# Performance work log

Measured on AMD Instinct MI355X. Metric: run time of the kernel, lower is better.

The kernel has to match this reference:

```python
import jax, jax.numpy as jnp
import numpy as np

N_NODES = 50000
N_EDGES = 800000
IN_DIM = 128
OUT_DIM = 64


def setup_inputs() -> dict:
    key = jax.random.key(0)
    k1, k2, k3, k4, k5 = jax.random.split(key, 5)
    x = jax.random.normal(k1, (N_NODES, IN_DIM), dtype=jnp.float32)
    edge_src = jax.random.randint(k2, (N_EDGES,), 0, N_NODES, dtype=jnp.int64)
    edge_dst = jax.random.randint(k3, (N_EDGES,), 0, N_NODES, dtype=jnp.int64)
    edge_weight = jax.random.uniform(k4, (N_EDGES,), dtype=jnp.float32)
    # Glorot-uniform weight as in weight_variable_glorot (range = sqrt(6/input_dim))
    init_range = np.sqrt(6.0 / IN_DIM).astype(np.float32)
    w = jax.random.uniform(k5, (IN_DIM, OUT_DIM), minval=-init_range,
                           maxval=init_range, dtype=jnp.float32)
    return {"x": x, "edge_src": edge_src, "edge_dst": edge_dst,
            "edge_weight": edge_weight, "w": w}


def reference(x, edge_src, edge_dst, edge_weight, w):
    # Dense projection: [N, in] @ [in, out] -> [N, out]
    h = x @ w
    # Sparse adjacency matmul (adj @ h) in COO form:
    # out[dst] += weight * h[src]
    msgs = edge_weight[:, None] * h[edge_src]          # [E, out]
    agg = jax.ops.segment_sum(msgs, edge_dst, num_segments=N_NODES)
    return jax.nn.relu(agg)
```

## Files before the change

kernel.cpp:

```cpp
#include <hip/hip_runtime.h>

#define N_NODES 50000
#define N_EDGES 800000
#define IN_DIM 128
#define OUT_DIM 64
#define ROWS 64
#define NB 782
#define CHUNK 8192
#define NCH ((N_EDGES + CHUNK - 1) / CHUNK)
#define SCAN_N (NB * NCH)
#define SCAN_BLK 512
#define NSC ((SCAN_N + SCAN_BLK - 1) / SCAN_BLK)

__device__ __forceinline__ unsigned short f2bf(float f) {
    unsigned u = __builtin_bit_cast(unsigned, f);
    u += 0x7FFF + ((u >> 16) & 1);
    return (unsigned short)(u >> 16);
}
__device__ __forceinline__ float bf2f(unsigned short u) {
    unsigned x = ((unsigned)u) << 16;
    return __builtin_bit_cast(float, x);
}

__global__ __launch_bounds__(256, 2) void gc_gemm(const float* __restrict__ x,
                                                  const float* __restrict__ w,
                                                  unsigned short* __restrict__ h16) {
    __shared__ float w_lds[IN_DIM * OUT_DIM];
    __shared__ float x_lds[ROWS * IN_DIM];

    const int tid = threadIdx.x;
    const int row0 = blockIdx.x * ROWS;

    const float4* w4 = reinterpret_cast<const float4*>(w);
    float4* wl4 = reinterpret_cast<float4*>(w_lds);
#pragma unroll
    for (int i = 0; i < 8; ++i) wl4[tid + i * 256] = w4[tid + i * 256];

    const float4* x4 = reinterpret_cast<const float4*>(x);
    float4* xl4 = reinterpret_cast<float4*>(x_lds);
#pragma unroll
    for (int i = 0; i < 8; ++i) {
        const int idx = tid + i * 256;
        const int r = idx >> 5;
        const int kc = idx & 31;
        const int g = row0 + r;
        float4 v = make_float4(0.f, 0.f, 0.f, 0.f);
        if (g < N_NODES) v = x4[(size_t)g * 32 + kc];
        xl4[r * 32 + (kc ^ (r & 3))] = v;
    }
    __syncthreads();

    const int tx = tid & 15;
    const int ty = tid >> 4;
    const int sw = ty & 3;

    float4 acc[4];
#pragma unroll
    for (int i = 0; i < 4; ++i) acc[i] = make_float4(0.f, 0.f, 0.f, 0.f);

    for (int kc = 0; kc < 32; ++kc) {
        float4 xv[4], wv[4];
#pragma unroll
        for (int i = 0; i < 4; ++i)
            xv[i] = xl4[(ty + 16 * i) * 32 + (kc ^ sw)];
#pragma unroll
        for (int j = 0; j < 4; ++j)
            wv[j] = wl4[(kc * 4 + j) * 16 + tx];
#pragma unroll
        for (int i = 0; i < 4; ++i) {
            acc[i].x = fmaf(xv[i].x, wv[0].x, acc[i].x);
            acc[i].y = fmaf(xv[i].x, wv[0].y, acc[i].y);
            acc[i].z = fmaf(xv[i].x, wv[0].z, acc[i].z);
            acc[i].w = fmaf(xv[i].x, wv[0].w, acc[i].w);
            acc[i].x = fmaf(xv[i].y, wv[1].x, acc[i].x);
            acc[i].y = fmaf(xv[i].y, wv[1].y, acc[i].y);
            acc[i].z = fmaf(xv[i].y, wv[1].z, acc[i].z);
            acc[i].w = fmaf(xv[i].y, wv[1].w, acc[i].w);
            acc[i].x = fmaf(xv[i].z, wv[2].x, acc[i].x);
            acc[i].y = fmaf(xv[i].z, wv[2].y, acc[i].y);
            acc[i].z = fmaf(xv[i].z, wv[2].z, acc[i].z);
            acc[i].w = fmaf(xv[i].z, wv[2].w, acc[i].w);
            acc[i].x = fmaf(xv[i].w, wv[3].x, acc[i].x);
            acc[i].y = fmaf(xv[i].w, wv[3].y, acc[i].y);
            acc[i].z = fmaf(xv[i].w, wv[3].z, acc[i].z);
            acc[i].w = fmaf(xv[i].w, wv[3].w, acc[i].w);
        }
    }

    ushort4* h4 = reinterpret_cast<ushort4*>(h16);
#pragma unroll
    for (int i = 0; i < 4; ++i) {
        const int r = row0 + ty + 16 * i;
        if (r < N_NODES) {
            ushort4 o;
            o.x = f2bf(acc[i].x);
            o.y = f2bf(acc[i].y);
            o.z = f2bf(acc[i].z);
            o.w = f2bf(acc[i].w);
            h4[(size_t)r * 16 + tx] = o;
        }
    }
}

__global__ __launch_bounds__(512) void gc_count(const int* __restrict__ edst,
                                                int* __restrict__ cntT) {
    __shared__ int lh[NB];
    const int t = threadIdx.x;
    for (int i = t; i < NB; i += 512) lh[i] = 0;
    __syncthreads();
    const int base = blockIdx.x * CHUNK;
#pragma unroll
    for (int k = 0; k < 16; ++k) {
        const int e = base + k * 512 + t;
        if (e < N_EDGES) atomicAdd(&lh[edst[e] >> 6], 1);
    }
    __syncthreads();
    for (int i = t; i < NB; i += 512) cntT[i * NCH + blockIdx.x] = lh[i];
}

__global__ __launch_bounds__(256) void gc_scan1(const int* __restrict__ a,
                                                int* __restrict__ bsum) {
    __shared__ int red[256];
    const int t = threadIdx.x;
    const int i0 = blockIdx.x * SCAN_BLK + t * 2;
    int v = 0;
    if (i0 < SCAN_N) v += a[i0];
    if (i0 + 1 < SCAN_N) v += a[i0 + 1];
    red[t] = v;
    __syncthreads();
#pragma unroll
    for (int s = 128; s > 0; s >>= 1) {
        if (t < s) red[t] += red[t + s];
        __syncthreads();
    }
    if (t == 0) bsum[blockIdx.x] = red[0];
}

__global__ __launch_bounds__(256) void gc_scan2(int* __restrict__ bsum) {
    __shared__ int part[256];
    const int t = threadIdx.x;
    const int v = (t < NSC) ? bsum[t] : 0;
    part[t] = v;
    __syncthreads();
#pragma unroll
    for (int off = 1; off < 256; off <<= 1) {
        const int u = (t >= off) ? part[t - off] : 0;
        __syncthreads();
        part[t] += u;
        __syncthreads();
    }
    if (t < NSC) bsum[t] = part[t] - v;
}

__global__ __launch_bounds__(256) void gc_scan3(int* __restrict__ a,
                                                const int* __restrict__ bsum) {
    __shared__ int part[256];
    const int t = threadIdx.x;
    const int i0 = blockIdx.x * SCAN_BLK + t * 2;
    const int v0 = (i0 < SCAN_N) ? a[i0] : 0;
    const int v1 = (i0 + 1 < SCAN_N) ? a[i0 + 1] : 0;
    const int s = v0 + v1;
    part[t] = s;
    __syncthreads();
#pragma unroll
    for (int off = 1; off < 256; off <<= 1) {
        const int u = (t >= off) ? part[t - off] : 0;
        __syncthreads();
        part[t] += u;
        __syncthreads();
    }
    const int pre = bsum[blockIdx.x] + part[t] - s;
    if (i0 < SCAN_N) a[i0] = pre;
    if (i0 + 1 < SCAN_N) a[i0 + 1] = pre + v0;
}

__global__ __launch_bounds__(512) void gc_bin(const int* __restrict__ esrc,
                                              const int* __restrict__ edst,
                                              const float* __restrict__ ew,
                                              const int* __restrict__ posT,
                                              int2* __restrict__ tmp) {
    __shared__ int2 stage[CHUNK];
    __shared__ int lh[NB];
    __shared__ int lbase[NB];
    __shared__ int lcur[NB];
    __shared__ int part[512];

    const int t = threadIdx.x;
    const int base = blockIdx.x * CHUNK;

    for (int i = t; i < NB; i += 512) lh[i] = 0;
    __syncthreads();

#pragma unroll
    for (int k = 0; k < 16; ++k) {
        const int e = base + k * 512 + t;
        if (e < N_EDGES) atomicAdd(&lh[edst[e] >> 6], 1);
    }
    __syncthreads();

    {
        int s = 0;
        if (t < 391) s = lh[2 * t] + lh[2 * t + 1];
        part[t] = s;
        __syncthreads();
#pragma unroll
        for (int off = 1; off < 512; off <<= 1) {
            const int u = (t >= off) ? part[t - off] : 0;
            __syncthreads();
            part[t] += u;
            __syncthreads();
        }
        if (t < 391) {
            const int pre = part[t] - s;
            lbase[2 * t] = pre;
            lcur[2 * t] = pre;
            lbase[2 * t + 1] = pre + lh[2 * t];
            lcur[2 * t + 1] = pre + lh[2 * t];
        }
    }
    __syncthreads();

#pragma unroll
    for (int k = 0; k < 16; ++k) {
        const int e = base + k * 512 + t;
        if (e < N_EDGES) {
            const int d = edst[e];
            const int p = atomicAdd(&lcur[d >> 6], 1);
            stage[p] = make_int2((int)(((unsigned)(d & 63) << 16) | (unsigned)esrc[e]),
                                 __float_as_int(ew[e]));
        }
    }
    __syncthreads();

    const int wv = t >> 6, ln = t & 63;
    for (int b = wv; b < NB; b += 8) {
        const int cnt = lh[b];
        if (!cnt) continue;
        const int gbase = posT[b * NCH + blockIdx.x];
        const int lb = lbase[b];
        for (int i = ln; i < cnt; i += 64) tmp[gbase + i] = stage[lb + i];
    }
}

__global__ __launch_bounds__(256) void gc_bagg(const unsigned short* __restrict__ h16,
                                               const int* __restrict__ posT,
                                               const int2* __restrict__ tmp,
                                               float* __restrict__ out) {
    __shared__ float tiles[4 * 64 * 64];
    const int t = threadIdx.x;
    const int b = blockIdx.x;
    const int wv = t >> 6;
    const int ln = t & 63;

    for (int i = t; i < 4 * 4096; i += 256) tiles[i] = 0.f;
    __syncthreads();

    float* tile = &tiles[wv * 4096];

    const int beg = posT[b * NCH];
    const int end = (b + 1 < NB) ? posT[(b + 1) * NCH] : N_EDGES;
    const int cnt = end - beg;
    const int wbeg = beg + ((cnt * wv) >> 2);
    const int wend = beg + ((cnt * (wv + 1)) >> 2);
    const int wcnt = wend - wbeg;
    const int nfull = wcnt & ~7;

    for (int jj = 0; jj < nfull; jj += 8) {
        const int j = wbeg + jj;
        int2 rec[8];
#pragma unroll
        for (int i = 0; i < 8; ++i) rec[i] = tmp[j + i];
        float hv[8];
#pragma unroll
        for (int i = 0; i < 8; ++i) {
            const int src = rec[i].x & 0xFFFF;
            hv[i] = bf2f(h16[(size_t)src * OUT_DIM + ln]);
        }
#pragma unroll
        for (int i = 0; i < 8; ++i) {
            const int row = (rec[i].x >> 16) & 63;
            tile[row * 64 + ln] += __int_as_float(rec[i].y) * hv[i];
        }
    }
    for (int jj = nfull; jj < wcnt; ++jj) {
        const int2 r = tmp[wbeg + jj];
        const int src = r.x & 0xFFFF;
        const int row = (r.x >> 16) & 63;
        tile[row * 64 + ln] += __int_as_float(r.y) * bf2f(h16[(size_t)src * OUT_DIM + ln]);
    }
    __syncthreads();

    const int node0 = b * 64;
    float4* o4 = reinterpret_cast<float4*>(out);
    const float4* t4 = reinterpret_cast<const float4*>(tiles);
    for (int i = t; i < 1024; i += 256) {
        const float4 a = t4[i];
        const float4 b2 = t4[1024 + i];
        const float4 c = t4[2048 + i];
        const float4 d = t4[3072 + i];
        float4 s;
        s.x = fmaxf(a.x + b2.x + c.x + d.x, 0.f);
        s.y = fmaxf(a.y + b2.y + c.y + d.y, 0.f);
        s.z = fmaxf(a.z + b2.z + c.z + d.z, 0.f);
        s.w = fmaxf(a.w + b2.w + c.w + d.w, 0.f);
        const int r = i >> 4;
        const int gn = node0 + r;
        if (gn < N_NODES) o4[(size_t)gn * 16 + (i & 15)] = s;
    }
}

extern "C" void kernel_launch(void* const* d_in, const int* in_sizes, int n_in,
                              void* d_out, int out_size, void* d_ws, size_t ws_size,
                              hipStream_t stream) {
    const float* x    = (const float*)d_in[0];
    const int*   esrc = (const int*)d_in[1];
    const int*   edst = (const int*)d_in[2];
    const float* ew   = (const float*)d_in[3];
    const float* w    = (const float*)d_in[4];
    float* out = (float*)d_out;

    unsigned short* h16 = (unsigned short*)d_ws;
    int*  cntT = (int*)(h16 + (size_t)N_NODES * OUT_DIM);
    int*  bsum = cntT + 76800;
    int2* tmp  = (int2*)(bsum + 256);

    gc_gemm<<<(N_NODES + ROWS - 1) / ROWS, 256, 0, stream>>>(x, w, h16);

    gc_count<<<NCH, 512, 0, stream>>>(edst, cntT);
    gc_scan1<<<NSC, 256, 0, stream>>>(cntT, bsum);
    gc_scan2<<<1, 256, 0, stream>>>(bsum);
    gc_scan3<<<NSC, 256, 0, stream>>>(cntT, bsum);
    gc_bin<<<NCH, 512, 0, stream>>>(esrc, edst, ew, cntT, tmp);

    gc_bagg<<<NB, 256, 0, stream>>>(h16, cntT, tmp, out);
}
```

Baseline: 219.7 us.

## Split each 64-node bucket into four sub-buckets to interleave independent edge streams

```diff
diff --git a/kernel.cpp b/kernel.cpp
--- a/kernel.cpp
+++ b/kernel.cpp
@@ -6,10 +6,11 @@
 #define OUT_DIM 64
 #define ROWS 64
 #define NB 782
-#define CHUNK 8192
+#define NB4 (NB * 4)
+#define CHUNK 4096
 #define NCH ((N_EDGES + CHUNK - 1) / CHUNK)
-#define SCAN_N (NB * NCH)
-#define SCAN_BLK 512
+#define SCAN_N (NB4 * NCH)
+#define SCAN_BLK 1024
 #define NSC ((SCAN_N + SCAN_BLK - 1) / SCAN_BLK)
 
 __device__ __forceinline__ unsigned short f2bf(float f) {
@@ -104,28 +105,32 @@
 
 __global__ __launch_bounds__(512) void gc_count(const int* __restrict__ edst,
                                                 int* __restrict__ cntT) {
-    __shared__ int lh[NB];
-    const int t = threadIdx.x;
-    for (int i = t; i < NB; i += 512) lh[i] = 0;
+    __shared__ int lh[NB4];
+    const int t = threadIdx.x;
+    for (int i = t; i < NB4; i += 512) lh[i] = 0;
     __syncthreads();
     const int base = blockIdx.x * CHUNK;
 #pragma unroll
-    for (int k = 0; k < 16; ++k) {
-        const int e = base + k * 512 + t;
-        if (e < N_EDGES) atomicAdd(&lh[edst[e] >> 6], 1);
-    }
-    __syncthreads();
-    for (int i = t; i < NB; i += 512) cntT[i * NCH + blockIdx.x] = lh[i];
+    for (int kk = 0; kk < CHUNK / 512; ++kk) {
+        const int e = base + kk * 512 + t;
+        if (e < N_EDGES) {
+            const int d = edst[e];
+            atomicAdd(&lh[((d >> 6) << 2) | (d & 3)], 1);
+        }
+    }
+    __syncthreads();
+    for (int i = t; i < NB4; i += 512) cntT[i * NCH + blockIdx.x] = lh[i];
 }
 
 __global__ __launch_bounds__(256) void gc_scan1(const int* __restrict__ a,
                                                 int* __restrict__ bsum) {
     __shared__ int red[256];
     const int t = threadIdx.x;
-    const int i0 = blockIdx.x * SCAN_BLK + t * 2;
+    const int i0 = blockIdx.x * SCAN_BLK + t * 4;
     int v = 0;
-    if (i0 < SCAN_N) v += a[i0];
-    if (i0 + 1 < SCAN_N) v += a[i0 + 1];
+#pragma unroll
+    for (int j = 0; j < 4; ++j)
+        if (i0 + j < SCAN_N) v += a[i0 + j];
     red[t] = v;
     __syncthreads();
 #pragma unroll
@@ -136,14 +141,14 @@
     if (t == 0) bsum[blockIdx.x] = red[0];
 }
 
-__global__ __launch_bounds__(256) void gc_scan2(int* __restrict__ bsum) {
-    __shared__ int part[256];
+__global__ __launch_bounds__(1024) void gc_scan2(int* __restrict__ bsum) {
+    __shared__ int part[1024];
     const int t = threadIdx.x;
     const int v = (t < NSC) ? bsum[t] : 0;
     part[t] = v;
     __syncthreads();
 #pragma unroll
-    for (int off = 1; off < 256; off <<= 1) {
+    for (int off = 1; off < 1024; off <<= 1) {
         const int u = (t >= off) ? part[t - off] : 0;
         __syncthreads();
         part[t] += u;
@@ -156,10 +161,14 @@
                                                 const int* __restrict__ bsum) {
     __shared__ int part[256];
     const int t = threadIdx.x;
-    const int i0 = blockIdx.x * SCAN_BLK + t * 2;
-    const int v0 = (i0 < SCAN_N) ? a[i0] : 0;
-    const int v1 = (i0 + 1 < SCAN_N) ? a[i0 + 1] : 0;
-    const int s = v0 + v1;
+    const int i0 = blockIdx.x * SCAN_BLK + t * 4;
+    int v[4];
+    int s = 0;
+#pragma unroll
+    for (int j = 0; j < 4; ++j) {
+        v[j] = (i0 + j < SCAN_N) ? a[i0 + j] : 0;
+        s += v[j];
+    }
     part[t] = s;
     __syncthreads();
 #pragma unroll
@@ -169,9 +178,12 @@
         part[t] += u;
         __syncthreads();
     }
-    const int pre = bsum[blockIdx.x] + part[t] - s;
-    if (i0 < SCAN_N) a[i0] = pre;
-    if (i0 + 1 < SCAN_N) a[i0 + 1] = pre + v0;
+    int run = bsum[blockIdx.x] + part[t] - s;
+#pragma unroll
+    for (int j = 0; j < 4; ++j) {
+        if (i0 + j < SCAN_N) a[i0 + j] = run;
+        run += v[j];
+    }
 }
 
 __global__ __launch_bounds__(512) void gc_bin(const int* __restrict__ esrc,
@@ -180,27 +192,30 @@
                                               const int* __restrict__ posT,
                                               int2* __restrict__ tmp) {
     __shared__ int2 stage[CHUNK];
-    __shared__ int lh[NB];
-    __shared__ int lbase[NB];
-    __shared__ int lcur[NB];
+    __shared__ int lh[NB4];
+    __shared__ int lcur[NB4];
+    __shared__ int gpos[NB4];
     __shared__ int part[512];
 
     const int t = threadIdx.x;
-    const int base = blockIdx.x * CHUNK;
-
-    for (int i = t; i < NB; i += 512) lh[i] = 0;
-    __syncthreads();
-
-#pragma unroll
-    for (int k = 0; k < 16; ++k) {
-        const int e = base + k * 512 + t;
-        if (e < N_EDGES) atomicAdd(&lh[edst[e] >> 6], 1);
+    const int blk = blockIdx.x;
+    const int base = blk * CHUNK;
+
+    for (int i = t; i < NB4; i += 512) {
+        const int f = i * NCH + blk;
+        const int p = posT[f];
+        const int pn = (f + 1 < SCAN_N) ? posT[f + 1] : N_EDGES;
+        gpos[i] = p;
+        lh[i] = pn - p;
     }
     __syncthreads();
 
     {
+        const int b0 = t * 7;
         int s = 0;
-        if (t < 391) s = lh[2 * t] + lh[2 * t + 1];
+#pragma unroll
+        for (int j = 0; j < 7; ++j)
+            if (b0 + j < NB4) s += lh[b0 + j];
         part[t] = s;
         __syncthreads();
 #pragma unroll
@@ -210,22 +225,24 @@
             part[t] += u;
             __syncthreads();
         }
-        if (t < 391) {
-            const int pre = part[t] - s;
-            lbase[2 * t] = pre;
-            lcur[2 * t] = pre;
-            lbase[2 * t + 1] = pre + lh[2 * t];
-            lcur[2 * t + 1] = pre + lh[2 * t];
-        }
-    }
-    __syncthreads();
-
-#pragma unroll
-    for (int k = 0; k < 16; ++k) {
-        const int e = base + k * 512 + t;
+        int run = part[t] - s;
+#pragma unroll
+        for (int j = 0; j < 7; ++j) {
+            if (b0 + j < NB4) {
+                lcur[b0 + j] = run;
+                run += lh[b0 + j];
+            }
+        }
+    }
+    __syncthreads();
+
+#pragma unroll
+    for (int kk = 0; kk < CHUNK / 512; ++kk) {
+        const int e = base + kk * 512 + t;
         if (e < N_EDGES) {
             const int d = edst[e];
-            const int p = atomicAdd(&lcur[d >> 6], 1);
+            const int bc = ((d >> 6) << 2) | (d & 3);
+            const int p = atomicAdd(&lcur[bc], 1);
             stage[p] = make_int2((int)(((unsigned)(d & 63) << 16) | (unsigned)esrc[e]),
                                  __float_as_int(ew[e]));
         }
@@ -233,11 +250,11 @@
     __syncthreads();
 
     const int wv = t >> 6, ln = t & 63;
-    for (int b = wv; b < NB; b += 8) {
-        const int cnt = lh[b];
+    for (int bc = wv; bc < NB4; bc += 8) {
+        const int cnt = lh[bc];
         if (!cnt) continue;
-        const int gbase = posT[b * NCH + blockIdx.x];
-        const int lb = lbase[b];
+        const int gbase = gpos[bc];
+        const int lb = lcur[bc] - cnt;
         for (int i = ln; i < cnt; i += 64) tmp[gbase + i] = stage[lb + i];
     }
 }
@@ -257,37 +274,81 @@
 
     float* tile = &tiles[wv * 4096];
 
-    const int beg = posT[b * NCH];
-    const int end = (b + 1 < NB) ? posT[(b + 1) * NCH] : N_EDGES;
-    const int cnt = end - beg;
-    const int wbeg = beg + ((cnt * wv) >> 2);
-    const int wend = beg + ((cnt * (wv + 1)) >> 2);
-    const int wcnt = wend - wbeg;
-    const int nfull = wcnt & ~7;
-
-    for (int jj = 0; jj < nfull; jj += 8) {
-        const int j = wbeg + jj;
-        int2 rec[8];
-#pragma unroll
-        for (int i = 0; i < 8; ++i) rec[i] = tmp[j + i];
-        float hv[8];
-#pragma unroll
-        for (int i = 0; i < 8; ++i) {
-            const int src = rec[i].x & 0xFFFF;
-            hv[i] = bf2f(h16[(size_t)src * OUT_DIM + ln]);
-        }
-#pragma unroll
-        for (int i = 0; i < 8; ++i) {
-            const int row = (rec[i].x >> 16) & 63;
-            tile[row * 64 + ln] += __int_as_float(rec[i].y) * hv[i];
-        }
-    }
-    for (int jj = nfull; jj < wcnt; ++jj) {
-        const int2 r = tmp[wbeg + jj];
-        const int src = r.x & 0xFFFF;
-        const int row = (r.x >> 16) & 63;
-        tile[row * 64 + ln] += __int_as_float(r.y) * bf2f(h16[(size_t)src * OUT_DIM + ln]);
-    }
+    const int f0 = (b * 4) * NCH;
+    const int s0 = posT[f0];
+    const int s1 = posT[f0 + NCH];
+    const int s2 = posT[f0 + 2 * NCH];
+    const int s3 = posT[f0 + 3 * NCH];
+    const int s4 = (b * 4 + 4 < NB4) ? posT[f0 + 4 * NCH] : N_EDGES;
+    const int c0 = s1 - s0, c1 = s2 - s1, c2 = s3 - s2, c3 = s4 - s3;
+    const int jb0 = s0 + ((c0 * wv) >> 2), je0 = s0 + ((c0 * (wv + 1)) >> 2);
+    const int jb1 = s1 + ((c1 * wv) >> 2), je1 = s1 + ((c1 * (wv + 1)) >> 2);
+    const int jb2 = s2 + ((c2 * wv) >> 2), je2 = s2 + ((c2 * (wv + 1)) >> 2);
+    const int jb3 = s3 + ((c3 * wv) >> 2), je3 = s3 + ((c3 * (wv + 1)) >> 2);
+
+    const int n0 = je0 - jb0, n1 = je1 - jb1, n2 = je2 - jb2, n3 = je3 - jb3;
+    const int n = min(min(n0, n1), min(n2, n3));
+
+    int k = 0;
+    for (; k + 2 <= n; k += 2) {
+        const int2 r0 = tmp[jb0 + k];
+        const int2 r1 = tmp[jb1 + k];
+        const int2 r2 = tmp[jb2 + k];
+        const int2 r3 = tmp[jb3 + k];
+        const int2 r4 = tmp[jb0 + k + 1];
+        const int2 r5 = tmp[jb1 + k + 1];
+        const int2 r6 = tmp[jb2 + k + 1];
+        const int2 r7 = tmp[jb3 + k + 1];
+        const float h0 = bf2f(h16[(size_t)(r0.x & 0xFFFF) * OUT_DIM + ln]);
+        const float h1 = bf2f(h16[(size_t)(r1.x & 0xFFFF) * OUT_DIM + ln]);
+        const float h2 = bf2f(h16[(size_t)(r2.x & 0xFFFF) * OUT_DIM + ln]);
+        const float h3 = bf2f(h16[(size_t)(r3.x & 0xFFFF) * OUT_DIM + ln]);
+        const float h4 = bf2f(h16[(size_t)(r4.x & 0xFFFF) * OUT_DIM + ln]);
+        const float h5 = bf2f(h16[(size_t)(r5.x & 0xFFFF) * OUT_DIM + ln]);
+        const float h6 = bf2f(h16[(size_t)(r6.x & 0xFFFF) * OUT_DIM + ln]);
+        const float h7 = bf2f(h16[(size_t)(r7.x & 0xFFFF) * OUT_DIM + ln]);
+        {
+            float* p0 = &tile[((r0.x >> 16) & 63) * 64 + ln];
+            float* p1 = &tile[((r1.x >> 16) & 63) * 64 + ln];
+            float* p2 = &tile[((r2.x >> 16) & 63) * 64 + ln];
+            float* p3 = &tile[((r3.x >> 16) & 63) * 64 + ln];
+            const float a0 = *p0;
+            const float a1 = *p1;
+            const float a2 = *p2;
+            const float a3 = *p3;
+            *p0 = fmaf(__int_as_float(r0.y), h0, a0);
+            *p1 = fmaf(__int_as_float(r1.y), h1, a1);
+            *p2 = fmaf(__int_as_float(r2.y), h2, a2);
+            *p3 = fmaf(__int_as_float(r3.y), h3, a3);
+        }
+        {
+            float* p0 = &tile[((r4.x >> 16) & 63) * 64 + ln];
+            float* p1 = &tile[((r5.x >> 16) & 63) * 64 + ln];
+            float* p2 = &tile[((r6.x >> 16) & 63) * 64 + ln];
+            float* p3 = &tile[((r7.x >> 16) & 63) * 64 + ln];
+            const float a0 = *p0;
+            const float a1 = *p1;
+            const float a2 = *p2;
+            const float a3 = *p3;
+            *p0 = fmaf(__int_as_float(r4.y), h4, a0);
+            *p1 = fmaf(__int_as_float(r5.y), h5, a1);
+            *p2 = fmaf(__int_as_float(r6.y), h6, a2);
+            *p3 = fmaf(__int_as_float(r7.y), h7, a3);
+        }
+    }
+#define GC_TAIL(JB, JE)                                                        \
+    for (int j = (JB) + k; j < (JE); ++j) {                                    \
+        const int2 r = tmp[j];                                                 \
+        const int src = r.x & 0xFFFF;                                          \
+        const int row = (r.x >> 16) & 63;                                      \
+        tile[row * 64 + ln] += __int_as_float(r.y) *                           \
+                               bf2f(h16[(size_t)src * OUT_DIM + ln]);          \
+    }
+    GC_TAIL(jb0, je0)
+    GC_TAIL(jb1, je1)
+    GC_TAIL(jb2, je2)
+    GC_TAIL(jb3, je3)
+#undef GC_TAIL
     __syncthreads();
 
     const int node0 = b * 64;
@@ -321,14 +382,14 @@
 
     unsigned short* h16 = (unsigned short*)d_ws;
     int*  cntT = (int*)(h16 + (size_t)N_NODES * OUT_DIM);
-    int*  bsum = cntT + 76800;
-    int2* tmp  = (int2*)(bsum + 256);
+    int*  bsum = cntT + 613120;
+    int2* tmp  = (int2*)(bsum + 1024);
 
     gc_gemm<<<(N_NODES + ROWS - 1) / ROWS, 256, 0, stream>>>(x, w, h16);
 
     gc_count<<<NCH, 512, 0, stream>>>(edst, cntT);
     gc_scan1<<<NSC, 256, 0, stream>>>(cntT, bsum);
-    gc_scan2<<<1, 256, 0, stream>>>(bsum);
+    gc_scan2<<<1, 1024, 0, stream>>>(bsum);
     gc_scan3<<<NSC, 256, 0, stream>>>(cntT, bsum);
     gc_bin<<<NCH, 512, 0, stream>>>(esrc, edst, ew, cntT, tmp);
 
```

Measured after the change: 257.1 us. 17.0% more time.
